# Performance work log

Measured on AMD Instinct MI355X. Metric: run time of the kernel, lower is better.

Reference implementation:

```python
import jax, jax.numpy as jnp
import numpy as np

S, N, M, D = 4, 4096, 4096, 128
NEG = -1e30
EPS = 1e-12


def setup_inputs() -> dict:
    key = jax.random.key(0)
    k1, k2, k3 = jax.random.split(key, 3)
    art = jax.random.normal(k1, (S, N, D), dtype=jnp.float32)
    ref = jax.random.normal(k2, (S, M, D), dtype=jnp.float32)
    pos_mask = jax.random.randint(k3, (S, N, M), 0, 2).astype(jnp.bool_)
    log_temperature = jnp.log(jnp.asarray(0.01, dtype=jnp.float32))
    return {"art": art, "ref": ref, "pos_mask": pos_mask, "log_temperature": log_temperature}


def _l2norm(x):
    # F.normalize: x / max(||x||, eps)
    n = jnp.sqrt(jnp.sum(x * x, axis=-1, keepdims=True))
    return x / jnp.maximum(n, EPS)


def reference(art, ref, pos_mask, log_temperature):
    temp = jnp.exp(log_temperature)
    a = _l2norm(art)                                   # [S,N,D]
    r = _l2norm(ref)                                   # [S,M,D]
    logits = jnp.einsum("snd,smd->snm", a, r) / temp   # [S,N,M]

    den = jax.nn.logsumexp(logits, axis=-1)                              # [S,N]
    num = jax.nn.logsumexp(jnp.where(pos_mask, logits, NEG), axis=-1)    # [S,N]

    n_pos = jnp.sum(pos_mask, axis=-1)                 # [S,N]
    n_ref = logits.shape[-1]
    valid = (n_pos > 0) & (n_ref > n_pos)              # skip anchors with 0 pos or all pos

    per_anchor = den - num                             # -(num - den)
    cnt = jnp.sum(valid, axis=-1)                      # [S]
    stem_loss = jnp.sum(jnp.where(valid, per_anchor, 0.0), axis=-1) / jnp.maximum(cnt, 1)
    stem_valid = cnt > 0
    loss = jnp.sum(jnp.where(stem_valid, stem_loss, 0.0)) / jnp.maximum(jnp.sum(stem_valid), 1)
    return loss
```

## Files before the change

### kernel.cpp

```cpp
#include <hip/hip_runtime.h>
#include <hip/hip_bf16.h>
#include <math.h>

#define S_ 4
#define N_ 4096
#define M_ 4096
#define D_ 128
#define NEG_ (-1e30f)
#define CH_ 4
#define MCH_ (M_ / CH_)
#define LN2_ 0.69314718055994531f
#define LOG2E_ 1.44269504088896340f

typedef __bf16 bf16x8 __attribute__((ext_vector_type(8)));
typedef float f32x4 __attribute__((ext_vector_type(4)));

__device__ __forceinline__ unsigned short f2bf(float f) {
    unsigned u = __float_as_uint(f);
    unsigned r = (u + 0x7FFFu + ((u >> 16) & 1u)) >> 16;
    return (unsigned short)r;
}

__global__ void nrm_rows_kernel(const float* __restrict__ art, const float* __restrict__ ref,
                                unsigned short* __restrict__ an, unsigned short* __restrict__ rn) {
    const int w = threadIdx.x >> 6;
    const int lane = threadIdx.x & 63;
    const int row = blockIdx.x * 4 + w;
    const bool is_art = row < S_ * N_;
    const float* src = is_art ? (art + (size_t)row * D_)
                              : (ref + (size_t)(row - S_ * N_) * D_);
    unsigned short* dst = is_art ? (an + (size_t)row * D_)
                                 : (rn + (size_t)(row - S_ * N_) * D_);
    const float2 v = *reinterpret_cast<const float2*>(src + lane * 2);
    float ss = v.x * v.x + v.y * v.y;
#pragma unroll
    for (int off = 1; off < 64; off <<= 1) ss += __shfl_xor(ss, off);
    const float scale = 1.0f / fmaxf(sqrtf(ss), 1e-12f);
    unsigned pack = (unsigned)f2bf(v.x * scale) | ((unsigned)f2bf(v.y * scale) << 16);
    *reinterpret_cast<unsigned*>(dst + lane * 2) = pack;
}

template <bool BYTE>
__device__ __forceinline__ void lse_loop(
    const unsigned short* __restrict__ rbase, const void* __restrict__ maskp,
    size_t melt0, const bf16x8* __restrict__ bfr, float scale2,
    float& dmax, float& dsum, float& nsum, float& npf) {
#pragma unroll 2
    for (int it = 0; it < (MCH_ / 2) / 64; ++it) {
        float fpm[16];
#pragma unroll
        for (int t = 0; t < 4; ++t) {
            if (BYTE) {
                const uchar4 mv = *reinterpret_cast<const uchar4*>(
                    (const unsigned char*)maskp + melt0 + it * 64 + t * 16);
                fpm[t * 4 + 0] = (float)mv.x; fpm[t * 4 + 1] = (float)mv.y;
                fpm[t * 4 + 2] = (float)mv.z; fpm[t * 4 + 3] = (float)mv.w;
            } else {
                const int4 mv = *reinterpret_cast<const int4*>(
                    (const int*)maskp + melt0 + it * 64 + t * 16);
                fpm[t * 4 + 0] = (float)mv.x; fpm[t * 4 + 1] = (float)mv.y;
                fpm[t * 4 + 2] = (float)mv.z; fpm[t * 4 + 3] = (float)mv.w;
            }
        }
        f32x4 acc0 = {0.f, 0.f, 0.f, 0.f}, acc1 = {0.f, 0.f, 0.f, 0.f};
        f32x4 acc2 = {0.f, 0.f, 0.f, 0.f}, acc3 = {0.f, 0.f, 0.f, 0.f};
        const unsigned short* rp = rbase + (size_t)it * 64 * D_;
#pragma unroll
        for (int kc = 0; kc < 4; ++kc) {
            acc0 = __builtin_amdgcn_mfma_f32_16x16x32_bf16(
                *reinterpret_cast<const bf16x8*>(rp + 0 * 16 * D_ + kc * 32), bfr[kc], acc0, 0, 0, 0);
            acc1 = __builtin_amdgcn_mfma_f32_16x16x32_bf16(
                *reinterpret_cast<const bf16x8*>(rp + 1 * 16 * D_ + kc * 32), bfr[kc], acc1, 0, 0, 0);
            acc2 = __builtin_amdgcn_mfma_f32_16x16x32_bf16(
                *reinterpret_cast<const bf16x8*>(rp + 2 * 16 * D_ + kc * 32), bfr[kc], acc2, 0, 0, 0);
            acc3 = __builtin_amdgcn_mfma_f32_16x16x32_bf16(
                *reinterpret_cast<const bf16x8*>(rp + 3 * 16 * D_ + kc * 32), bfr[kc], acc3, 0, 0, 0);
        }
        float l[16];
#pragma unroll
        for (int i = 0; i < 4; ++i) {
            l[i]      = acc0[i] * scale2;  l[4 + i]  = acc1[i] * scale2;
            l[8 + i]  = acc2[i] * scale2;  l[12 + i] = acc3[i] * scale2;
        }
        float a0 = fmaxf(l[0], l[1]),  a1 = fmaxf(l[2], l[3]);
        float a2 = fmaxf(l[4], l[5]),  a3 = fmaxf(l[6], l[7]);
        float a4 = fmaxf(l[8], l[9]),  a5 = fmaxf(l[10], l[11]);
        float a6 = fmaxf(l[12], l[13]), a7 = fmaxf(l[14], l[15]);
        float b0 = fmaxf(a0, a1), b1 = fmaxf(a2, a3), b2 = fmaxf(a4, a5), b3 = fmaxf(a6, a7);
        float tmax = fmaxf(fmaxf(b0, b1), fmaxf(b2, b3));
        const float nmx = fmaxf(dmax, tmax);
        const float r = exp2f(dmax - nmx);
        float e[16];
#pragma unroll
        for (int i = 0; i < 16; ++i) e[i] = exp2f(l[i] - nmx);
        float s0 = (e[0] + e[1]) + (e[2] + e[3]), s1 = (e[4] + e[5]) + (e[6] + e[7]);
        float s2 = (e[8] + e[9]) + (e[10] + e[11]), s3 = (e[12] + e[13]) + (e[14] + e[15]);
        dsum = dsum * r + ((s0 + s1) + (s2 + s3));
        float p0 = fpm[0] * e[0], p1 = fpm[1] * e[1], p2 = fpm[2] * e[2], p3 = fpm[3] * e[3];
#pragma unroll
        for (int i = 4; i < 16; i += 4) {
            p0 = fmaf(fpm[i], e[i], p0);     p1 = fmaf(fpm[i + 1], e[i + 1], p1);
            p2 = fmaf(fpm[i + 2], e[i + 2], p2); p3 = fmaf(fpm[i + 3], e[i + 3], p3);
        }
        nsum = nsum * r + ((p0 + p1) + (p2 + p3));
        float q0 = (fpm[0] + fpm[1]) + (fpm[2] + fpm[3]), q1 = (fpm[4] + fpm[5]) + (fpm[6] + fpm[7]);
        float q2 = (fpm[8] + fpm[9]) + (fpm[10] + fpm[11]), q3 = (fpm[12] + fpm[13]) + (fpm[14] + fpm[15]);
        npf += ((q0 + q1) + (q2 + q3));
        dmax = nmx;
    }
}

__global__ __launch_bounds__(256, 4) void infonce_main_kernel(
    const unsigned short* __restrict__ an, const unsigned short* __restrict__ rn,
    const void* __restrict__ maskp, const float* __restrict__ logtemp,
    float4* __restrict__ part4) {

    const int bid = blockIdx.x;
    const int swz = (bid & 7) * 256 + (bid >> 3);
    const int ch = swz >> 9;
    const int s = (swz >> 7) & 3;
    const int nblk = swz & 127;
    const int n_base = nblk * 32;

    const int tid = threadIdx.x;
    const int w = tid >> 6;
    const int lane = tid & 63;
    const int nsub = w & 1;
    const int msub = w >> 1;
    const int n16 = n_base + nsub * 16;
    const int lrow = lane & 15;
    const int lgrp = lane >> 4;
    const float scale2 = __expf(-logtemp[0]) * LOG2E_;

    const unsigned probe = ((const unsigned*)maskp)[lane];
    const bool mask_is_byte = (__ballot(probe > 1u) != 0ull);

    bf16x8 bfr[4];
    const unsigned short* abase = an + ((size_t)(s * N_ + n16 + lrow)) * D_ + lgrp * 8;
#pragma unroll
    for (int kc = 0; kc < 4; ++kc)
        bfr[kc] = *reinterpret_cast<const bf16x8*>(abase + kc * 32);

    const int m_begin = ch * MCH_ + msub * (MCH_ / 2);
    const unsigned short* rbase = rn + ((size_t)(s * M_ + m_begin + lrow)) * D_ + lgrp * 8;
    const size_t melt0 = ((size_t)(s * N_ + n16 + lrow)) * M_ + m_begin + lgrp * 4;

    float dmax = NEG_, dsum = 0.f, nsum = 0.f, npf = 0.f;
    if (mask_is_byte) lse_loop<true >(rbase, maskp, melt0, bfr, scale2, dmax, dsum, nsum, npf);
    else              lse_loop<false>(rbase, maskp, melt0, bfr, scale2, dmax, dsum, nsum, npf);

#pragma unroll
    for (int off = 16; off < 64; off <<= 1) {
        float odm = __shfl_xor(dmax, off), ods = __shfl_xor(dsum, off);
        float ons = __shfl_xor(nsum, off), onp = __shfl_xor(npf, off);
        float nm = fmaxf(dmax, odm);
        float ra = exp2f(dmax - nm), rb = exp2f(odm - nm);
        dsum = dsum * ra + ods * rb;
        nsum = nsum * ra + ons * rb;
        npf += onp;
        dmax = nm;
    }

    __shared__ float4 lds4[4][16];
    if (lane < 16) lds4[w][lane] = make_float4(dmax, dsum, nsum, npf);
    __syncthreads();

    if (w == 0 && lane < 32) {
        const int wsub = lane >> 4;
        const int ni = lane & 15;
        const float4 A = lds4[wsub][ni];
        const float4 B = lds4[wsub + 2][ni];
        const float nm = fmaxf(A.x, B.x);
        const float ra = exp2f(A.x - nm), rb = exp2f(B.x - nm);
        const float ds = A.y * ra + B.y * rb;
        const float ns = A.z * ra + B.z * rb;
        const float np = A.w + B.w;
        const int ag = s * N_ + n_base + wsub * 16 + ni;
        part4[ag * CH_ + ch] = make_float4(nm, ds, ns, np);
    }
}

__global__ void reduce_kernel(const float4* __restrict__ part4, float2* __restrict__ bpart) {
    const int a = blockIdx.x * 256 + threadIdx.x;
    const int w = threadIdx.x >> 6;
    const int lane = threadIdx.x & 63;
    float dm = NEG_, ds = 0.f, ns = 0.f, npf = 0.f;
#pragma unroll
    for (int ch = 0; ch < CH_; ++ch) {
        const float4 p = part4[a * CH_ + ch];
        const float m2 = fmaxf(dm, p.x);
        const float ra = exp2f(dm - m2), rb = exp2f(p.x - m2);
        ds = ds * ra + p.y * rb;
        ns = ns * ra + p.z * rb;
        npf += p.w;
        dm = m2;
    }
    const bool valid = (npf > 0.5f) && (npf < (float)M_ - 0.5f);
    float pa = valid ? LN2_ * (log2f(ds) - log2f(ns)) : 0.f;
    float cv = valid ? 1.f : 0.f;
#pragma unroll
    for (int off = 1; off < 64; off <<= 1) {
        pa += __shfl_xor(pa, off);
        cv += __shfl_xor(cv, off);
    }
    __shared__ float sp[4], sc[4];
    if (lane == 0) { sp[w] = pa; sc[w] = cv; }
    __syncthreads();
    if (threadIdx.x == 0)
        bpart[blockIdx.x] = make_float2(sp[0] + sp[1] + sp[2] + sp[3],
                                        sc[0] + sc[1] + sc[2] + sc[3]);
}

__global__ void finalize_kernel(const float2* __restrict__ bpart, float* __restrict__ out) {
    const int t = threadIdx.x;
    const float2 v = bpart[t];
    float pa = v.x, cv = v.y;
#pragma unroll
    for (int off = 1; off < 16; off <<= 1) {
        pa += __shfl_xor(pa, off);
        cv += __shfl_xor(cv, off);
    }
    const float p0 = __shfl(pa, 0),  c0 = __shfl(cv, 0);
    const float p1 = __shfl(pa, 16), c1 = __shfl(cv, 16);
    const float p2 = __shfl(pa, 32), c2 = __shfl(cv, 32);
    const float p3 = __shfl(pa, 48), c3 = __shfl(cv, 48);
    if (t == 0) {
        float total = 0.f;
        int scnt = 0;
        const float ps[4] = {p0, p1, p2, p3};
        const float cs[4] = {c0, c1, c2, c3};
        for (int s = 0; s < S_; ++s) {
            const float stem = ps[s] / fmaxf(cs[s], 1.f);
            if (cs[s] > 0.f) { total += stem; scnt++; }
        }
        out[0] = total / (float)(scnt > 0 ? scnt : 1);
    }
}

extern "C" void kernel_launch(void* const* d_in, const int* in_sizes, int n_in,
                              void* d_out, int out_size, void* d_ws, size_t ws_size,
                              hipStream_t stream) {
    const float* art = (const float*)d_in[0];
    const float* ref = (const float*)d_in[1];
    const void* mask = d_in[2];
    const float* lt = (const float*)d_in[3];
    float* out = (float*)d_out;

    char* ws = (char*)d_ws;
    unsigned short* an = (unsigned short*)ws;
    unsigned short* rn = (unsigned short*)(ws + (size_t)4194304);
    float4* part4 = (float4*)(ws + (size_t)8388608);
    float2* bpart = (float2*)(ws + (size_t)9437184);

    nrm_rows_kernel<<<(S_ * (N_ + M_)) / 4, 256, 0, stream>>>(art, ref, an, rn);
    infonce_main_kernel<<<S_ * (N_ / 32) * CH_, 256, 0, stream>>>(an, rn, mask, lt, part4);
    reduce_kernel<<<(S_ * N_) / 256, 256, 0, stream>>>(part4, bpart);
    finalize_kernel<<<1, 64, 0, stream>>>(bpart, out);
}
```

Measured before the change: 461.2 us.

## Prepack positive mask into bitfield before the fused logsumexp kernel

Adds a separate kernel that streams the boolean or int mask once and packs it into 16-bit words, one bit per element. The main kernel then reads one 64-bit word per iteration instead of 16 bytes or ints per lane, selects exponentials with bit tests, and counts positives with popcount. The main kernel's occupancy hint is also raised. The extra pass still reads the full mask and writes the packed copy, so total mask traffic is not lower; the gain has to come from a leaner main loop and better occupancy.

```diff
diff --git a/kernel.cpp b/kernel.cpp
--- a/kernel.cpp
+++ b/kernel.cpp
@@ -11,6 +11,7 @@
 #define MCH_ (M_ / CH_)
 #define LN2_ 0.69314718055994531f
 #define LOG2E_ 1.44269504088896340f
+#define NWORDS_ (S_ * N_ * (M_ / 16))
 
 typedef __bf16 bf16x8 __attribute__((ext_vector_type(8)));
 typedef float f32x4 __attribute__((ext_vector_type(4)));
@@ -40,28 +41,80 @@
     *reinterpret_cast<unsigned*>(dst + lane * 2) = pack;
 }
 
-template <bool BYTE>
-__device__ __forceinline__ void lse_loop(
-    const unsigned short* __restrict__ rbase, const void* __restrict__ maskp,
-    size_t melt0, const bf16x8* __restrict__ bfr, float scale2,
-    float& dmax, float& dsum, float& nsum, float& npf) {
+__global__ __launch_bounds__(256) void bitpack_kernel(const unsigned* __restrict__ maskp,
+                                                      unsigned short* __restrict__ bits) {
+    const unsigned probe = maskp[threadIdx.x & 63];
+    const bool byte_mode = (__ballot(probe > 1u) != 0ull);
+    const int stride = gridDim.x * 256;
+    const int4* p = (const int4*)maskp;
+    if (byte_mode) {
+        for (int i = blockIdx.x * 256 + threadIdx.x; i < NWORDS_; i += stride) {
+            const int4 q = p[i];
+            unsigned v =  ((unsigned)q.x & 1u)         | ((((unsigned)q.x >> 8) & 1u) << 1)
+                       | ((((unsigned)q.x >> 16) & 1u) << 2) | ((((unsigned)q.x >> 24) & 1u) << 3)
+                       | (((unsigned)q.y & 1u) << 4)   | ((((unsigned)q.y >> 8) & 1u) << 5)
+                       | ((((unsigned)q.y >> 16) & 1u) << 6) | ((((unsigned)q.y >> 24) & 1u) << 7)
+                       | (((unsigned)q.z & 1u) << 8)   | ((((unsigned)q.z >> 8) & 1u) << 9)
+                       | ((((unsigned)q.z >> 16) & 1u) << 10) | ((((unsigned)q.z >> 24) & 1u) << 11)
+                       | (((unsigned)q.w & 1u) << 12)  | ((((unsigned)q.w >> 8) & 1u) << 13)
+                       | ((((unsigned)q.w >> 16) & 1u) << 14) | ((((unsigned)q.w >> 24) & 1u) << 15);
+            bits[i] = (unsigned short)v;
+        }
+    } else {
+        for (int i = blockIdx.x * 256 + threadIdx.x; i < NWORDS_; i += stride) {
+            const int4 a = p[i * 4 + 0], b = p[i * 4 + 1], c = p[i * 4 + 2], d = p[i * 4 + 3];
+            unsigned v =  ((unsigned)a.x & 1u)        | (((unsigned)a.y & 1u) << 1)
+                       | (((unsigned)a.z & 1u) << 2)  | (((unsigned)a.w & 1u) << 3)
+                       | (((unsigned)b.x & 1u) << 4)  | (((unsigned)b.y & 1u) << 5)
+                       | (((unsigned)b.z & 1u) << 6)  | (((unsigned)b.w & 1u) << 7)
+                       | (((unsigned)c.x & 1u) << 8)  | (((unsigned)c.y & 1u) << 9)
+                       | (((unsigned)c.z & 1u) << 10) | (((unsigned)c.w & 1u) << 11)
+                       | (((unsigned)d.x & 1u) << 12) | (((unsigned)d.y & 1u) << 13)
+                       | (((unsigned)d.z & 1u) << 14) | (((unsigned)d.w & 1u) << 15);
+            bits[i] = (unsigned short)v;
+        }
+    }
+}
+
+__global__ __launch_bounds__(256, 8) void infonce_main_kernel(
+    const unsigned short* __restrict__ an, const unsigned short* __restrict__ rn,
+    const unsigned long long* __restrict__ bits64, const float* __restrict__ logtemp,
+    float4* __restrict__ part4) {
+
+    const int bid = blockIdx.x;
+    const int swz = (bid & 7) * 256 + (bid >> 3);
+    const int ch = swz >> 9;
+    const int s = (swz >> 7) & 3;
+    const int nblk = swz & 127;
+    const int n_base = nblk * 32;
+
+    const int tid = threadIdx.x;
+    const int w = tid >> 6;
+    const int lane = tid & 63;
+    const int nsub = w & 1;
+    const int msub = w >> 1;
+    const int n16 = n_base + nsub * 16;
+    const int lrow = lane & 15;
+    const int lgrp = lane >> 4;
+    const float scale2 = __expf(-logtemp[0]) * LOG2E_;
+
+    bf16x8 bfr[4];
+    const unsigned short* abase = an + ((size_t)(s * N_ + n16 + lrow)) * D_ + lgrp * 8;
+#pragma unroll
+    for (int kc = 0; kc < 4; ++kc)
+        bfr[kc] = *reinterpret_cast<const bf16x8*>(abase + kc * 32);
+
+    const int m_begin = ch * MCH_ + msub * (MCH_ / 2);
+    const unsigned short* rbase = rn + ((size_t)(s * M_ + m_begin + lrow)) * D_ + lgrp * 8;
+    const unsigned long long* brow =
+        bits64 + (size_t)(s * N_ + n16 + lrow) * (M_ / 64) + (m_begin >> 6);
+
+    float dmax = NEG_, dsum = 0.f, nsum = 0.f;
+    int npos = 0;
+
 #pragma unroll 2
     for (int it = 0; it < (MCH_ / 2) / 64; ++it) {
-        float fpm[16];
-#pragma unroll
-        for (int t = 0; t < 4; ++t) {
-            if (BYTE) {
-                const uchar4 mv = *reinterpret_cast<const uchar4*>(
-                    (const unsigned char*)maskp + melt0 + it * 64 + t * 16);
-                fpm[t * 4 + 0] = (float)mv.x; fpm[t * 4 + 1] = (float)mv.y;
-                fpm[t * 4 + 2] = (float)mv.z; fpm[t * 4 + 3] = (float)mv.w;
-            } else {
-                const int4 mv = *reinterpret_cast<const int4*>(
-                    (const int*)maskp + melt0 + it * 64 + t * 16);
-                fpm[t * 4 + 0] = (float)mv.x; fpm[t * 4 + 1] = (float)mv.y;
-                fpm[t * 4 + 2] = (float)mv.z; fpm[t * 4 + 3] = (float)mv.w;
-            }
-        }
+        const unsigned long long w64 = brow[it];
         f32x4 acc0 = {0.f, 0.f, 0.f, 0.f}, acc1 = {0.f, 0.f, 0.f, 0.f};
         f32x4 acc2 = {0.f, 0.f, 0.f, 0.f}, acc3 = {0.f, 0.f, 0.f, 0.f};
         const unsigned short* rp = rbase + (size_t)it * 64 * D_;
@@ -76,6 +129,12 @@
             acc3 = __builtin_amdgcn_mfma_f32_16x16x32_bf16(
                 *reinterpret_cast<const bf16x8*>(rp + 3 * 16 * D_ + kc * 32), bfr[kc], acc3, 0, 0, 0);
         }
+        const unsigned long long v = w64 >> (lgrp * 4);
+        const unsigned nib0 = (unsigned)v & 0xFu;
+        const unsigned nib1 = (unsigned)(v >> 16) & 0xFu;
+        const unsigned nib2 = (unsigned)(v >> 32) & 0xFu;
+        const unsigned nib3 = (unsigned)(v >> 48) & 0xFu;
+        npos += __popc(nib0 | (nib1 << 4) | (nib2 << 8) | (nib3 << 12));
         float l[16];
 #pragma unroll
         for (int i = 0; i < 4; ++i) {
@@ -86,69 +145,29 @@
         float a2 = fmaxf(l[4], l[5]),  a3 = fmaxf(l[6], l[7]);
         float a4 = fmaxf(l[8], l[9]),  a5 = fmaxf(l[10], l[11]);
         float a6 = fmaxf(l[12], l[13]), a7 = fmaxf(l[14], l[15]);
-        float b0 = fmaxf(a0, a1), b1 = fmaxf(a2, a3), b2 = fmaxf(a4, a5), b3 = fmaxf(a6, a7);
-        float tmax = fmaxf(fmaxf(b0, b1), fmaxf(b2, b3));
+        float tmax = fmaxf(fmaxf(fmaxf(a0, a1), fmaxf(a2, a3)),
+                           fmaxf(fmaxf(a4, a5), fmaxf(a6, a7)));
         const float nmx = fmaxf(dmax, tmax);
         const float r = exp2f(dmax - nmx);
         float e[16];
 #pragma unroll
         for (int i = 0; i < 16; ++i) e[i] = exp2f(l[i] - nmx);
-        float s0 = (e[0] + e[1]) + (e[2] + e[3]), s1 = (e[4] + e[5]) + (e[6] + e[7]);
+        float s0 = (e[0] + e[1]) + (e[2] + e[3]),   s1 = (e[4] + e[5]) + (e[6] + e[7]);
         float s2 = (e[8] + e[9]) + (e[10] + e[11]), s3 = (e[12] + e[13]) + (e[14] + e[15]);
         dsum = dsum * r + ((s0 + s1) + (s2 + s3));
-        float p0 = fpm[0] * e[0], p1 = fpm[1] * e[1], p2 = fpm[2] * e[2], p3 = fpm[3] * e[3];
-#pragma unroll
-        for (int i = 4; i < 16; i += 4) {
-            p0 = fmaf(fpm[i], e[i], p0);     p1 = fmaf(fpm[i + 1], e[i + 1], p1);
-            p2 = fmaf(fpm[i + 2], e[i + 2], p2); p3 = fmaf(fpm[i + 3], e[i + 3], p3);
-        }
+        float p0 = ((nib0 & 1u)      ? e[0]  : 0.f) + (((nib0 >> 1) & 1u) ? e[1]  : 0.f)
+                 + (((nib0 >> 2) & 1u) ? e[2]  : 0.f) + (((nib0 >> 3) & 1u) ? e[3]  : 0.f);
+        float p1 = ((nib1 & 1u)      ? e[4]  : 0.f) + (((nib1 >> 1) & 1u) ? e[5]  : 0.f)
+                 + (((nib1 >> 2) & 1u) ? e[6]  : 0.f) + (((nib1 >> 3) & 1u) ? e[7]  : 0.f);
+        float p2 = ((nib2 & 1u)      ? e[8]  : 0.f) + (((nib2 >> 1) & 1u) ? e[9]  : 0.f)
+                 + (((nib2 >> 2) & 1u) ? e[10] : 0.f) + (((nib2 >> 3) & 1u) ? e[11] : 0.f);
+        float p3 = ((nib3 & 1u)      ? e[12] : 0.f) + (((nib3 >> 1) & 1u) ? e[13] : 0.f)
+                 + (((nib3 >> 2) & 1u) ? e[14] : 0.f) + (((nib3 >> 3) & 1u) ? e[15] : 0.f);
         nsum = nsum * r + ((p0 + p1) + (p2 + p3));
-        float q0 = (fpm[0] + fpm[1]) + (fpm[2] + fpm[3]), q1 = (fpm[4] + fpm[5]) + (fpm[6] + fpm[7]);
-        float q2 = (fpm[8] + fpm[9]) + (fpm[10] + fpm[11]), q3 = (fpm[12] + fpm[13]) + (fpm[14] + fpm[15]);
-        npf += ((q0 + q1) + (q2 + q3));
         dmax = nmx;
     }
-}
-
-__global__ __launch_bounds__(256, 4) void infonce_main_kernel(
-    const unsigned short* __restrict__ an, const unsigned short* __restrict__ rn,
-    const void* __restrict__ maskp, const float* __restrict__ logtemp,
-    float4* __restrict__ part4) {
-
-    const int bid = blockIdx.x;
-    const int swz = (bid & 7) * 256 + (bid >> 3);
-    const int ch = swz >> 9;
-    const int s = (swz >> 7) & 3;
-    const int nblk = swz & 127;
-    const int n_base = nblk * 32;
-
-    const int tid = threadIdx.x;
-    const int w = tid >> 6;
-    const int lane = tid & 63;
-    const int nsub = w & 1;
-    const int msub = w >> 1;
-    const int n16 = n_base + nsub * 16;
-    const int lrow = lane & 15;
-    const int lgrp = lane >> 4;
-    const float scale2 = __expf(-logtemp[0]) * LOG2E_;
-
-    const unsigned probe = ((const unsigned*)maskp)[lane];
-    const bool mask_is_byte = (__ballot(probe > 1u) != 0ull);
-
-    bf16x8 bfr[4];
-    const unsigned short* abase = an + ((size_t)(s * N_ + n16 + lrow)) * D_ + lgrp * 8;
-#pragma unroll
-    for (int kc = 0; kc < 4; ++kc)
-        bfr[kc] = *reinterpret_cast<const bf16x8*>(abase + kc * 32);
-
-    const int m_begin = ch * MCH_ + msub * (MCH_ / 2);
-    const unsigned short* rbase = rn + ((size_t)(s * M_ + m_begin + lrow)) * D_ + lgrp * 8;
-    const size_t melt0 = ((size_t)(s * N_ + n16 + lrow)) * M_ + m_begin + lgrp * 4;
-
-    float dmax = NEG_, dsum = 0.f, nsum = 0.f, npf = 0.f;
-    if (mask_is_byte) lse_loop<true >(rbase, maskp, melt0, bfr, scale2, dmax, dsum, nsum, npf);
-    else              lse_loop<false>(rbase, maskp, melt0, bfr, scale2, dmax, dsum, nsum, npf);
-
+
+    float npf = (float)npos;
 #pragma unroll
     for (int off = 16; off < 64; off <<= 1) {
         float odm = __shfl_xor(dmax, off), ods = __shfl_xor(dsum, off);
@@ -249,11 +268,14 @@
     char* ws = (char*)d_ws;
     unsigned short* an = (unsigned short*)ws;
     unsigned short* rn = (unsigned short*)(ws + (size_t)4194304);
-    float4* part4 = (float4*)(ws + (size_t)8388608);
-    float2* bpart = (float2*)(ws + (size_t)9437184);
+    unsigned short* bits = (unsigned short*)(ws + (size_t)8388608);
+    float4* part4 = (float4*)(ws + (size_t)16777216);
+    float2* bpart = (float2*)(ws + (size_t)17825792);
 
     nrm_rows_kernel<<<(S_ * (N_ + M_)) / 4, 256, 0, stream>>>(art, ref, an, rn);
-    infonce_main_kernel<<<S_ * (N_ / 32) * CH_, 256, 0, stream>>>(an, rn, mask, lt, part4);
+    bitpack_kernel<<<4096, 256, 0, stream>>>((const unsigned*)mask, bits);
+    infonce_main_kernel<<<S_ * (N_ / 32) * CH_, 256, 0, stream>>>(
+        an, rn, (const unsigned long long*)bits, lt, part4);
     reduce_kernel<<<(S_ * N_) / 256, 256, 0, stream>>>(part4, bpart);
     finalize_kernel<<<1, 64, 0, stream>>>(bpart, out);
 }
```

Measured after the change: 526.8 us. +14.2%, slower.
